# Optimization experiments

Hardware: AMD Instinct MI355X
Metric: run time of the kernel (lower is better)

## Reference

```python
import jax, jax.numpy as jnp
import numpy as np

H = W = 32
C = 384
NH = 12
HEAD = C // NH
SCALE = HEAD ** -0.5
WS = 8            # window size
SS = 4            # shift size
N = WS * WS       # tokens per window (64)
NW = (H // WS) * (W // WS)  # windows per image (16)
HIDDEN = 4 * C
EPS = 1e-5
SQRT_2_OVER_PI = float(np.sqrt(2.0 / np.pi))


def _relative_position_index():
    ch = np.arange(WS)
    coords = np.stack(np.meshgrid(ch, ch, indexing='ij')).reshape(2, -1)  # [2, N]
    rel = (coords[:, :, None] - coords[:, None, :]).transpose(1, 2, 0)    # [N, N, 2]
    rel[:, :, 0] += WS - 1
    rel[:, :, 1] += WS - 1
    rel[:, :, 0] *= 2 * WS - 1
    return rel.sum(-1)  # [N, N] int


def _attn_mask():
    img = np.zeros((H, W), np.float32)
    sl = (slice(0, -WS), slice(-WS, -SS), slice(-SS, None))
    cnt = 0
    for hs in sl:
        for ws_ in sl:
            img[hs, ws_] = cnt
            cnt += 1
    m = img.reshape(H // WS, WS, W // WS, WS).transpose(0, 2, 1, 3).reshape(-1, N)  # [nW, N]
    am = m[:, None, :] - m[:, :, None]
    return np.where(am != 0, -100.0, 0.0).astype(np.float32)  # [nW, N, N]


REL_IDX = jnp.asarray(_relative_position_index())
ATTN_MASK = jnp.asarray(_attn_mask())


def _gelu(x):
    return x * 0.5 * (1.0 + jnp.tanh(SQRT_2_OVER_PI * (x + 0.044715 * x ** 3)))


def _layernorm(x, g, b):
    mu = jnp.mean(x, axis=-1, keepdims=True)
    var = jnp.mean(jnp.square(x - mu), axis=-1, keepdims=True)
    return (x - mu) * jax.lax.rsqrt(var + EPS) * g + b


def _window_partition(x):  # [B,H,W,C] -> [B*nW, N, C]
    B = x.shape[0]
    x = x.reshape(B, H // WS, WS, W // WS, WS, C).transpose(0, 1, 3, 2, 4, 5)
    return x.reshape(-1, N, C)


def _window_reverse(w, B):  # [B*nW, N, C] -> [B,H,W,C]
    x = w.reshape(B, H // WS, W // WS, WS, WS, C).transpose(0, 1, 3, 2, 4, 5)
    return x.reshape(B, H, W, C)


def setup_inputs() -> dict:
    key = jax.random.key(0)
    ks = jax.random.split(key, 16)
    s = 0.02
    return {
        'x': jax.random.normal(ks[0], (32, H * W, C), jnp.float32),
        'norm1_g': jnp.ones((C,), jnp.float32),
        'norm1_b': jnp.zeros((C,), jnp.float32),
        'qkv_w': jax.random.normal(ks[1], (C, 3 * C), jnp.float32) * s,
        'qkv_b': jnp.zeros((3 * C,), jnp.float32),
        'rel_bias_table': jax.random.normal(ks[2], ((2 * WS - 1) ** 2, NH), jnp.float32) * s,
        'proj_w': jax.random.normal(ks[3], (C, C), jnp.float32) * s,
        'proj_b': jnp.zeros((C,), jnp.float32),
        'norm2_g': jnp.ones((C,), jnp.float32),
        'norm2_b': jnp.zeros((C,), jnp.float32),
        'fc1_w': jax.random.normal(ks[4], (C, HIDDEN), jnp.float32) * s,
        'fc1_b': jnp.zeros((HIDDEN,), jnp.float32),
        'fc2_w': jax.random.normal(ks[5], (HIDDEN, C), jnp.float32) * s,
        'fc2_b': jnp.zeros((C,), jnp.float32),
    }


def reference(x, norm1_g, norm1_b, qkv_w, qkv_b, rel_bias_table, proj_w, proj_b,
              norm2_g, norm2_b, fc1_w, fc1_b, fc2_w, fc2_b):
    B = x.shape[0]
    shortcut = x
    y = _layernorm(x, norm1_g, norm1_b).reshape(B, H, W, C)
    y = jnp.roll(y, shift=(-SS, -SS), axis=(1, 2))          # cyclic shift
    win = _window_partition(y)                               # [B*nW, N, C]

    qkv = (win @ qkv_w + qkv_b).reshape(-1, N, 3, NH, HEAD).transpose(2, 0, 3, 1, 4)
    q, k, v = qkv[0], qkv[1], qkv[2]                         # [B*nW, NH, N, HEAD]
    attn = jnp.einsum('whnd,whmd->whnm', q * SCALE, k)       # [B*nW, NH, N, N]

    bias = rel_bias_table[REL_IDX.reshape(-1)].reshape(N, N, NH).transpose(2, 0, 1)
    attn = attn + bias[None]
    attn = attn.reshape(B, NW, NH, N, N) + ATTN_MASK[None, :, None]
    attn = jax.nn.softmax(attn.reshape(-1, NH, N, N), axis=-1)

    out = jnp.einsum('whnm,whmd->wnhd', attn, v).reshape(-1, N, C)
    out = out @ proj_w + proj_b                              # [B*nW, N, C]

    y = _window_reverse(out, B)
    y = jnp.roll(y, shift=(SS, SS), axis=(1, 2)).reshape(B, H * W, C)

    x = shortcut + y                                         # drop_path is identity (eval)
    h = _layernorm(x, norm2_g, norm2_b)
    h = _gelu(h @ fc1_w + fc1_b) @ fc2_w + fc2_b
    return x + h
```

## Files before the change

kernel.cpp:

```cpp
#include <hip/hip_runtime.h>
#include <hip/hip_bf16.h>
#include <math.h>

typedef __hip_bfloat16 bf16;
typedef __attribute__((ext_vector_type(8))) short short8;
typedef __attribute__((ext_vector_type(4))) float floatx4;

static constexpr int TOK = 32768;
static constexpr int CDIM = 384;
static constexpr int HID = 1536;

__device__ __forceinline__ bf16 f2bf(float v) { return __float2bfloat16(v); }

__device__ __forceinline__ void unpack8(uint4 u, float* f) {
  f[0] = __uint_as_float(u.x << 16); f[1] = __uint_as_float(u.x & 0xffff0000u);
  f[2] = __uint_as_float(u.y << 16); f[3] = __uint_as_float(u.y & 0xffff0000u);
  f[4] = __uint_as_float(u.z << 16); f[5] = __uint_as_float(u.z & 0xffff0000u);
  f[6] = __uint_as_float(u.w << 16); f[7] = __uint_as_float(u.w & 0xffff0000u);
}

__device__ __forceinline__ unsigned short bf_bits(float a) {
  bf16 h = __float2bfloat16(a);
  unsigned short u;
  __builtin_memcpy(&u, &h, 2);
  return u;
}
__device__ __forceinline__ unsigned pack2(float a, float b) {
  return (unsigned)bf_bits(a) | ((unsigned)bf_bits(b) << 16);
}

typedef const __attribute__((address_space(1))) unsigned gas_t;
typedef __attribute__((address_space(3))) unsigned las_t;
__device__ __forceinline__ void gload16(const bf16* g, const bf16* l) {
  __builtin_amdgcn_global_load_lds((gas_t*)g, (las_t*)l, 16, 0, 0);
}

__global__ void k_convt(const float* __restrict__ src, bf16* __restrict__ dst,
                        int Kd, int Nd) {
  int tid = blockIdx.x * 256 + threadIdx.x;
  if (tid >= Kd * Nd) return;
  int k = tid / Nd, n = tid - k * Nd;
  dst[(size_t)n * Kd + k] = f2bf(src[tid]);
}

__global__ __launch_bounds__(256) void k_ln1(const float* __restrict__ x,
                                             const float* __restrict__ g,
                                             const float* __restrict__ b,
                                             bf16* __restrict__ out) {
  int wt = blockIdx.x * 4 + (threadIdx.x >> 6);
  int lane = threadIdx.x & 63;
  int win = wt >> 6, ntok = wt & 63;
  int bimg = win >> 4, wi = win & 15;
  int sh = (((wi >> 2) << 3) + (ntok >> 3) + 4) & 31;
  int sw = (((wi & 3) << 3) + (ntok & 7) + 4) & 31;
  const float* xr = x + ((size_t)bimg * 1024 + sh * 32 + sw) * CDIM;
  float v[6]; float s = 0.f, ss = 0.f;
#pragma unroll
  for (int j = 0; j < 6; ++j) {
    float t = xr[j * 64 + lane];
    v[j] = t; s += t; ss += t * t;
  }
#pragma unroll
  for (int off = 32; off > 0; off >>= 1) {
    s += __shfl_xor(s, off, 64);
    ss += __shfl_xor(ss, off, 64);
  }
  float mu = s * (1.f / 384.f);
  float var = ss * (1.f / 384.f) - mu * mu;
  float rs = rsqrtf(var + 1e-5f);
  bf16* orow = out + (size_t)wt * CDIM;
#pragma unroll
  for (int j = 0; j < 6; ++j) {
    int c = j * 64 + lane;
    orow[c] = f2bf((v[j] - mu) * rs * g[c] + b[c]);
  }
}

__global__ __launch_bounds__(256) void k_ln2(const float* __restrict__ x1,
                                             const float* __restrict__ g,
                                             const float* __restrict__ b,
                                             bf16* __restrict__ out) {
  int t = blockIdx.x * 4 + (threadIdx.x >> 6);
  int lane = threadIdx.x & 63;
  const float* xr = x1 + (size_t)t * CDIM;
  float v[6]; float s = 0.f, ss = 0.f;
#pragma unroll
  for (int j = 0; j < 6; ++j) {
    float q = xr[j * 64 + lane];
    v[j] = q; s += q; ss += q * q;
  }
#pragma unroll
  for (int off = 32; off > 0; off >>= 1) {
    s += __shfl_xor(s, off, 64);
    ss += __shfl_xor(ss, off, 64);
  }
  float mu = s * (1.f / 384.f);
  float var = ss * (1.f / 384.f) - mu * mu;
  float rs = rsqrtf(var + 1e-5f);
  bf16* orow = out + (size_t)t * CDIM;
#pragma unroll
  for (int j = 0; j < 6; ++j) {
    int c = j * 64 + lane;
    orow[c] = f2bf((v[j] - mu) * rs * g[c] + b[c]);
  }
}

template <int K, int EPI, int NT>
__global__ __launch_bounds__(256) void k_gemm(const bf16* __restrict__ A,
                                              const bf16* __restrict__ Bt,
                                              const float* __restrict__ bias,
                                              const float* __restrict__ extra,
                                              void* __restrict__ outp) {
  __shared__ __attribute__((aligned(16))) char pool[32768];
  bf16* As = (bf16*)pool;
  bf16* Bs = (bf16*)(pool + 16384);

  const int tid = threadIdx.x;
  const int wv = tid >> 6, lane = tid & 63;

  const int flat = blockIdx.x;
  const int xcd = flat & 7;
  const int idx = flat >> 3;
  const int rpx = (gridDim.x >> 3) / NT;
  const int cb = idx % NT;
  const int rb = idx / NT;
  const int mblk = (xcd * rpx + rb) * 128, nblk = cb * 128;

  const int srow = lane >> 3;
  const int scol8 = (lane & 7) ^ srow;
  const bf16* gaw = A + (size_t)(mblk + wv * 32 + srow) * K + scol8 * 8;
  const bf16* gbw = Bt + (size_t)(nblk + wv * 32 + srow) * K + scol8 * 8;
  const bf16* lAw = As + wv * 2048;
  const bf16* lBw = Bs + wv * 2048;

  const int wr = wv >> 1, wc = wv & 1;
  const int mr = lane & 15, q = lane >> 4;
  const bf16* faRow = As + (wr * 64 + mr) * 64;
  const bf16* fbRow = Bs + (wc * 64 + mr) * 64;
  const int sw0 = (q ^ (mr & 7)) * 8;
  const int sw4 = ((q + 4) ^ (mr & 7)) * 8;

  floatx4 acc[4][4];
#pragma unroll
  for (int i = 0; i < 4; ++i)
#pragma unroll
    for (int j = 0; j < 4; ++j) acc[i][j] = floatx4{0.f, 0.f, 0.f, 0.f};

  for (int k0 = 0; k0 < K; k0 += 64) {
    __syncthreads();
#pragma unroll
    for (int c = 0; c < 4; ++c) gload16(gaw + k0 + c * 8 * K, lAw + c * 512);
#pragma unroll
    for (int c = 0; c < 4; ++c) gload16(gbw + k0 + c * 8 * K, lBw + c * 512);
    __syncthreads();
    {
      short8 a[4], b[4];
#pragma unroll
      for (int mt = 0; mt < 4; ++mt) a[mt] = *(const short8*)(faRow + mt * 1024 + sw0);
#pragma unroll
      for (int nt = 0; nt < 4; ++nt) b[nt] = *(const short8*)(fbRow + nt * 1024 + sw0);
#pragma unroll
      for (int mt = 0; mt < 4; ++mt)
#pragma unroll
        for (int nt = 0; nt < 4; ++nt)
          acc[mt][nt] = __builtin_amdgcn_mfma_f32_16x16x32_bf16(a[mt], b[nt], acc[mt][nt], 0, 0, 0);
    }
    {
      short8 a[4], b[4];
#pragma unroll
      for (int mt = 0; mt < 4; ++mt) a[mt] = *(const short8*)(faRow + mt * 1024 + sw4);
#pragma unroll
      for (int nt = 0; nt < 4; ++nt) b[nt] = *(const short8*)(fbRow + nt * 1024 + sw4);
#pragma unroll
      for (int mt = 0; mt < 4; ++mt)
#pragma unroll
        for (int nt = 0; nt < 4; ++nt)
          acc[mt][nt] = __builtin_amdgcn_mfma_f32_16x16x32_bf16(a[mt], b[nt], acc[mt][nt], 0, 0, 0);
    }
  }

  __syncthreads();
  float* epsw = (float*)pool + wv * (16 * 68);
  const int rr = lane >> 2, c0 = (lane & 3) * 16;
#pragma unroll
  for (int mt = 0; mt < 4; ++mt) {
#pragma unroll
    for (int nt = 0; nt < 4; ++nt)
#pragma unroll
      for (int r = 0; r < 4; ++r)
        epsw[(q * 4 + r) * 68 + nt * 16 + mr] = acc[mt][nt][r];
    float v[16];
#pragma unroll
    for (int j = 0; j < 4; ++j) {
      float4 t = *(const float4*)&epsw[rr * 68 + c0 + j * 4];
      v[j * 4 + 0] = t.x; v[j * 4 + 1] = t.y; v[j * 4 + 2] = t.z; v[j * 4 + 3] = t.w;
    }
    const int grow = mblk + wr * 64 + mt * 16 + rr;
    const int gcol = nblk + wc * 64 + c0;

    if constexpr (EPI == 0) {
      int win = grow >> 6, ntok = grow & 63;
      int s = gcol / 384;
      int rem = gcol - s * 384;
      int h = rem >> 5, d0 = rem & 31;
      bf16* op = (bf16*)outp + (((size_t)s * 512 + win) * 12 + h) * 2048 + ntok * 32 + d0;
      uint4 pk;
      float bv[16];
#pragma unroll
      for (int j = 0; j < 16; ++j) bv[j] = v[j] + bias[gcol + j];
      pk.x = pack2(bv[0], bv[1]); pk.y = pack2(bv[2], bv[3]);
      pk.z = pack2(bv[4], bv[5]); pk.w = pack2(bv[6], bv[7]);
      *(uint4*)op = pk;
      pk.x = pack2(bv[8], bv[9]); pk.y = pack2(bv[10], bv[11]);
      pk.z = pack2(bv[12], bv[13]); pk.w = pack2(bv[14], bv[15]);
      *(uint4*)(op + 8) = pk;
    } else if constexpr (EPI == 1) {
      int win = grow >> 6, ntok = grow & 63;
      int bimg = win >> 4, wi = win & 15;
      int hh = (((wi >> 2) << 3) + (ntok >> 3) + 4) & 31;
      int ww = (((wi & 3) << 3) + (ntok & 7) + 4) & 31;
      size_t t = (size_t)bimg * 1024 + hh * 32 + ww;
      float* op = (float*)outp + t * CDIM + gcol;
      const float* xr = extra + t * CDIM + gcol;
#pragma unroll
      for (int j = 0; j < 4; ++j) {
        float4 xv = *(const float4*)(xr + j * 4);
        float4 ov;
        ov.x = xv.x + v[j * 4 + 0] + bias[gcol + j * 4 + 0];
        ov.y = xv.y + v[j * 4 + 1] + bias[gcol + j * 4 + 1];
        ov.z = xv.z + v[j * 4 + 2] + bias[gcol + j * 4 + 2];
        ov.w = xv.w + v[j * 4 + 3] + bias[gcol + j * 4 + 3];
        *(float4*)(op + j * 4) = ov;
      }
    } else if constexpr (EPI == 2) {
      float gv[16];
#pragma unroll
      for (int j = 0; j < 16; ++j) {
        float z = v[j] + bias[gcol + j];
        float u = 0.7978845608028654f * (z + 0.044715f * z * z * z);
        gv[j] = z / (1.f + __expf(-2.f * u));
      }
      bf16* op = (bf16*)outp + (size_t)grow * HID + gcol;
      uint4 pk;
      pk.x = pack2(gv[0], gv[1]); pk.y = pack2(gv[2], gv[3]);
      pk.z = pack2(gv[4], gv[5]); pk.w = pack2(gv[6], gv[7]);
      *(uint4*)op = pk;
      pk.x = pack2(gv[8], gv[9]); pk.y = pack2(gv[10], gv[11]);
      pk.z = pack2(gv[12], gv[13]); pk.w = pack2(gv[14], gv[15]);
      *(uint4*)(op + 8) = pk;
    } else {
      float* op = (float*)outp + (size_t)grow * CDIM + gcol;
      const float* xr = extra + (size_t)grow * CDIM + gcol;
#pragma unroll
      for (int j = 0; j < 4; ++j) {
        float4 xv = *(const float4*)(xr + j * 4);
        float4 ov;
        ov.x = xv.x + v[j * 4 + 0] + bias[gcol + j * 4 + 0];
        ov.y = xv.y + v[j * 4 + 1] + bias[gcol + j * 4 + 1];
        ov.z = xv.z + v[j * 4 + 2] + bias[gcol + j * 4 + 2];
        ov.w = xv.w + v[j * 4 + 3] + bias[gcol + j * 4 + 3];
        *(float4*)(op + j * 4) = ov;
      }
    }
  }
}

__global__ __launch_bounds__(64) void k_attn(const bf16* __restrict__ qkv,
                                             const float* __restrict__ tblg,
                                             bf16* __restrict__ out) {
  __shared__ __attribute__((aligned(16))) float ks[64][36];
  __shared__ __attribute__((aligned(16))) float vs[64][36];
  __shared__ float tbl[228];
  int bid = blockIdx.x;
  int win = bid / 12, head = bid - win * 12;
  int lane = threadIdx.x;

  for (int i = lane; i < 225; i += 64) tbl[i] = tblg[i * 12 + head];

  size_t base = ((size_t)win * 12 + head) * 2048 + lane * 32;
  const uint4* qp = (const uint4*)(qkv + base);
  const uint4* kp = (const uint4*)(qkv + (size_t)12582912 + base);
  const uint4* vp = (const uint4*)(qkv + (size_t)25165824 + base);

  float qreg[32];
#pragma unroll
  for (int i = 0; i < 4; ++i) { uint4 u = qp[i]; unpack8(u, qreg + i * 8); }
#pragma unroll
  for (int i = 0; i < 4; ++i) {
    uint4 u = kp[i]; float f[8]; unpack8(u, f);
    *(float4*)&ks[lane][i * 8] = make_float4(f[0], f[1], f[2], f[3]);
    *(float4*)&ks[lane][i * 8 + 4] = make_float4(f[4], f[5], f[6], f[7]);
  }
#pragma unroll
  for (int i = 0; i < 4; ++i) {
    uint4 u = vp[i]; float f[8]; unpack8(u, f);
    *(float4*)&vs[lane][i * 8] = make_float4(f[0], f[1], f[2], f[3]);
    *(float4*)&vs[lane][i * 8 + 4] = make_float4(f[4], f[5], f[6], f[7]);
  }

  int wi = win & 15;
  int r_i = lane >> 3, c_i = lane & 7;
  int rh = ((wi >> 2) << 3) + r_i, rw = ((wi & 3) << 3) + c_i;
  int rid = (rh < 24 ? 0 : (rh < 28 ? 1 : 2)) * 3 + (rw < 24 ? 0 : (rw < 28 ? 1 : 2));
  unsigned long long mask = 0;
#pragma unroll
  for (int v = 0; v < 9; ++v) {
    unsigned long long bb = __ballot(rid == v);
    if (rid == v) mask = bb;
  }
  const int base_i = r_i * 15 + c_i;
  __syncthreads();

  float o[32];
#pragma unroll
  for (int d = 0; d < 32; ++d) o[d] = 0.f;
  float l = 0.f;
#pragma unroll 2
  for (int j = 0; j < 64; ++j) {
    const float4* kr = (const float4*)ks[j];
    float dot = 0.f;
#pragma unroll
    for (int d4 = 0; d4 < 8; ++d4) {
      float4 kk = kr[d4];
      dot += qreg[d4 * 4 + 0] * kk.x;
      dot += qreg[d4 * 4 + 1] * kk.y;
      dot += qreg[d4 * 4 + 2] * kk.z;
      dot += qreg[d4 * 4 + 3] * kk.w;
    }
    int off_j = 112 - (j >> 3) * 15 - (j & 7);
    float bias = tbl[base_i + off_j];
    float madd = ((mask >> j) & 1ull) ? 0.f : -100.f;
    float p = __expf(dot * 0.17677669529663687f + bias + madd);
    l += p;
    const float4* vr = (const float4*)vs[j];
#pragma unroll
    for (int d4 = 0; d4 < 8; ++d4) {
      float4 vv = vr[d4];
      o[d4 * 4 + 0] += p * vv.x;
      o[d4 * 4 + 1] += p * vv.y;
      o[d4 * 4 + 2] += p * vv.z;
      o[d4 * 4 + 3] += p * vv.w;
    }
  }
  float inv = 1.f / l;
  uint4* o4 = (uint4*)(out + ((size_t)win * 64 + lane) * CDIM + head * 32);
#pragma unroll
  for (int i = 0; i < 4; ++i) {
    uint4 pk;
    pk.x = pack2(o[i * 8 + 0] * inv, o[i * 8 + 1] * inv);
    pk.y = pack2(o[i * 8 + 2] * inv, o[i * 8 + 3] * inv);
    pk.z = pack2(o[i * 8 + 4] * inv, o[i * 8 + 5] * inv);
    pk.w = pack2(o[i * 8 + 6] * inv, o[i * 8 + 7] * inv);
    o4[i] = pk;
  }
}

extern "C" void kernel_launch(void* const* d_in, const int* in_sizes, int n_in,
                              void* d_out, int out_size, void* d_ws, size_t ws_size,
                              hipStream_t stream) {
  const float* x = (const float*)d_in[0];
  const float* n1g = (const float*)d_in[1];
  const float* n1b = (const float*)d_in[2];
  const float* qkv_w = (const float*)d_in[3];
  const float* qkv_b = (const float*)d_in[4];
  const float* reltbl = (const float*)d_in[5];
  const float* proj_w = (const float*)d_in[6];
  const float* proj_b = (const float*)d_in[7];
  const float* n2g = (const float*)d_in[8];
  const float* n2b = (const float*)d_in[9];
  const float* fc1_w = (const float*)d_in[10];
  const float* fc1_b = (const float*)d_in[11];
  const float* fc2_w = (const float*)d_in[12];
  const float* fc2_b = (const float*)d_in[13];
  float* out = (float*)d_out;

  char* p = (char*)d_ws;
  bf16* w_qkv_t = (bf16*)p;  p += (size_t)442368 * 2;
  bf16* w_proj_t = (bf16*)p; p += (size_t)147456 * 2;
  bf16* w_fc1_t = (bf16*)p;  p += (size_t)589824 * 2;
  bf16* w_fc2_t = (bf16*)p;  p += (size_t)589824 * 2;
  bf16* bufA = (bf16*)p;     p += (size_t)12582912 * 2;
  bf16* qkvb = (bf16*)p;     p += (size_t)37748736 * 2;
  bf16* attno = (bf16*)p;    p += (size_t)12582912 * 2;
  float* x1 = (float*)p;     p += (size_t)12582912 * 4;
  bf16* hidden = qkvb;

  k_convt<<<dim3((442368 + 255) / 256), dim3(256), 0, stream>>>(qkv_w, w_qkv_t, 384, 1152);
  k_convt<<<dim3((147456 + 255) / 256), dim3(256), 0, stream>>>(proj_w, w_proj_t, 384, 384);
  k_convt<<<dim3((589824 + 255) / 256), dim3(256), 0, stream>>>(fc1_w, w_fc1_t, 384, 1536);
  k_convt<<<dim3((589824 + 255) / 256), dim3(256), 0, stream>>>(fc2_w, w_fc2_t, 1536, 384);

  k_ln1<<<dim3(8192), dim3(256), 0, stream>>>(x, n1g, n1b, bufA);
  k_gemm<384, 0, 9><<<dim3(9 * 256), dim3(256), 0, stream>>>(bufA, w_qkv_t, qkv_b, nullptr, qkvb);
  k_attn<<<dim3(6144), dim3(64), 0, stream>>>(qkvb, reltbl, attno);
  k_gemm<384, 1, 3><<<dim3(3 * 256), dim3(256), 0, stream>>>(attno, w_proj_t, proj_b, x, x1);
  k_ln2<<<dim3(8192), dim3(256), 0, stream>>>(x1, n2g, n2b, bufA);
  k_gemm<384, 2, 12><<<dim3(12 * 256), dim3(256), 0, stream>>>(bufA, w_fc1_t, fc1_b, nullptr, hidden);
  k_gemm<1536, 3, 3><<<dim3(3 * 256), dim3(256), 0, stream>>>(hidden, w_fc2_t, fc2_b, x1, out);
}
```

Measured before the change: 448.9 us.

## Rewrite window attention kernel with bf16 MFMA for QK^T and PV

The per-window attention kernel moves from per-lane scalar fp32 dot products over LDS-held K/V to bf16 MFMA 16x16x32 instructions for both the score and the output matmuls. Q, K and a transposed V are staged in LDS as bf16. Probabilities are written back to LDS as bf16, and row sums are reduced with shuffles. The aim is to cut the ALU-bound FMA work in attention, at the cost of bf16 rounding of the probabilities. Masked entries are zeroed directly instead of adding a -100 bias, and the code relies on single-wave ordering instead of barriers.

```diff
diff --git a/kernel.cpp b/kernel.cpp
--- a/kernel.cpp
+++ b/kernel.cpp
@@ -11,13 +11,6 @@
 static constexpr int HID = 1536;
 
 __device__ __forceinline__ bf16 f2bf(float v) { return __float2bfloat16(v); }
-
-__device__ __forceinline__ void unpack8(uint4 u, float* f) {
-  f[0] = __uint_as_float(u.x << 16); f[1] = __uint_as_float(u.x & 0xffff0000u);
-  f[2] = __uint_as_float(u.y << 16); f[3] = __uint_as_float(u.y & 0xffff0000u);
-  f[4] = __uint_as_float(u.z << 16); f[5] = __uint_as_float(u.z & 0xffff0000u);
-  f[6] = __uint_as_float(u.w << 16); f[7] = __uint_as_float(u.w & 0xffff0000u);
-}
 
 __device__ __forceinline__ unsigned short bf_bits(float a) {
   bf16 h = __float2bfloat16(a);
@@ -268,12 +261,19 @@
 __global__ __launch_bounds__(64) void k_attn(const bf16* __restrict__ qkv,
                                              const float* __restrict__ tblg,
                                              bf16* __restrict__ out) {
-  __shared__ __attribute__((aligned(16))) float ks[64][36];
-  __shared__ __attribute__((aligned(16))) float vs[64][36];
-  __shared__ float tbl[228];
-  int bid = blockIdx.x;
-  int win = bid / 12, head = bid - win * 12;
-  int lane = threadIdx.x;
+  __shared__ __attribute__((aligned(16))) char pool[16384];
+  bf16* Qs = (bf16*)pool;
+  bf16* Ks = (bf16*)(pool + 5120);
+  bf16* Ps = (bf16*)pool;
+  float* Os = (float*)pool;
+  bf16* Vt = (bf16*)(pool + 10240);
+  unsigned long long* msk = (unsigned long long*)(pool + 14848);
+  float* tbl = (float*)(pool + 15360);
+
+  const int bid = blockIdx.x;
+  const int win = bid / 12, head = bid - win * 12;
+  const int lane = threadIdx.x;
+  const int q = lane >> 4, mr = lane & 15;
 
   for (int i = lane; i < 225; i += 64) tbl[i] = tblg[i * 12 + head];
 
@@ -281,76 +281,131 @@
   const uint4* qp = (const uint4*)(qkv + base);
   const uint4* kp = (const uint4*)(qkv + (size_t)12582912 + base);
   const uint4* vp = (const uint4*)(qkv + (size_t)25165824 + base);
-
-  float qreg[32];
-#pragma unroll
-  for (int i = 0; i < 4; ++i) { uint4 u = qp[i]; unpack8(u, qreg + i * 8); }
-#pragma unroll
-  for (int i = 0; i < 4; ++i) {
-    uint4 u = kp[i]; float f[8]; unpack8(u, f);
-    *(float4*)&ks[lane][i * 8] = make_float4(f[0], f[1], f[2], f[3]);
-    *(float4*)&ks[lane][i * 8 + 4] = make_float4(f[4], f[5], f[6], f[7]);
-  }
-#pragma unroll
-  for (int i = 0; i < 4; ++i) {
-    uint4 u = vp[i]; float f[8]; unpack8(u, f);
-    *(float4*)&vs[lane][i * 8] = make_float4(f[0], f[1], f[2], f[3]);
-    *(float4*)&vs[lane][i * 8 + 4] = make_float4(f[4], f[5], f[6], f[7]);
-  }
-
-  int wi = win & 15;
-  int r_i = lane >> 3, c_i = lane & 7;
-  int rh = ((wi >> 2) << 3) + r_i, rw = ((wi & 3) << 3) + c_i;
-  int rid = (rh < 24 ? 0 : (rh < 28 ? 1 : 2)) * 3 + (rw < 24 ? 0 : (rw < 28 ? 1 : 2));
-  unsigned long long mask = 0;
-#pragma unroll
-  for (int v = 0; v < 9; ++v) {
-    unsigned long long bb = __ballot(rid == v);
-    if (rid == v) mask = bb;
-  }
-  const int base_i = r_i * 15 + c_i;
-  __syncthreads();
-
-  float o[32];
-#pragma unroll
-  for (int d = 0; d < 32; ++d) o[d] = 0.f;
-  float l = 0.f;
-#pragma unroll 2
-  for (int j = 0; j < 64; ++j) {
-    const float4* kr = (const float4*)ks[j];
-    float dot = 0.f;
-#pragma unroll
-    for (int d4 = 0; d4 < 8; ++d4) {
-      float4 kk = kr[d4];
-      dot += qreg[d4 * 4 + 0] * kk.x;
-      dot += qreg[d4 * 4 + 1] * kk.y;
-      dot += qreg[d4 * 4 + 2] * kk.z;
-      dot += qreg[d4 * 4 + 3] * kk.w;
-    }
-    int off_j = 112 - (j >> 3) * 15 - (j & 7);
-    float bias = tbl[base_i + off_j];
-    float madd = ((mask >> j) & 1ull) ? 0.f : -100.f;
-    float p = __expf(dot * 0.17677669529663687f + bias + madd);
-    l += p;
-    const float4* vr = (const float4*)vs[j];
-#pragma unroll
-    for (int d4 = 0; d4 < 8; ++d4) {
-      float4 vv = vr[d4];
-      o[d4 * 4 + 0] += p * vv.x;
-      o[d4 * 4 + 1] += p * vv.y;
-      o[d4 * 4 + 2] += p * vv.z;
-      o[d4 * 4 + 3] += p * vv.w;
-    }
-  }
-  float inv = 1.f / l;
+#pragma unroll
+  for (int i = 0; i < 4; ++i) *(uint4*)(Qs + lane * 40 + i * 8) = qp[i];
+#pragma unroll
+  for (int i = 0; i < 4; ++i) *(uint4*)(Ks + lane * 40 + i * 8) = kp[i];
+  {
+    union { uint4 u[4]; unsigned short h[32]; } vv;
+#pragma unroll
+    for (int i = 0; i < 4; ++i) vv.u[i] = vp[i];
+    unsigned short* VtU = (unsigned short*)Vt;
+#pragma unroll
+    for (int d = 0; d < 32; ++d) VtU[d * 72 + lane] = vv.h[d];
+  }
+  {
+    int wi = win & 15;
+    int ri = lane >> 3, ci = lane & 7;
+    int rh = ((wi >> 2) << 3) + ri, rw = ((wi & 3) << 3) + ci;
+    int rid = (rh < 24 ? 0 : (rh < 28 ? 1 : 2)) * 3 + (rw < 24 ? 0 : (rw < 28 ? 1 : 2));
+    unsigned long long m = 0;
+#pragma unroll
+    for (int v = 0; v < 9; ++v) {
+      unsigned long long bb = __ballot(rid == v);
+      if (rid == v) m = bb;
+    }
+    msk[lane] = m;
+  }
+
+  floatx4 sac[4][4];
+#pragma unroll
+  for (int i = 0; i < 4; ++i)
+#pragma unroll
+    for (int j = 0; j < 4; ++j) sac[i][j] = floatx4{0.f, 0.f, 0.f, 0.f};
+  {
+    short8 af[4], bf[4];
+#pragma unroll
+    for (int t = 0; t < 4; ++t) af[t] = *(const short8*)(Qs + (t * 16 + mr) * 40 + q * 8);
+#pragma unroll
+    for (int t = 0; t < 4; ++t) bf[t] = *(const short8*)(Ks + (t * 16 + mr) * 40 + q * 8);
+#pragma unroll
+    for (int mt = 0; mt < 4; ++mt)
+#pragma unroll
+      for (int nt = 0; nt < 4; ++nt)
+        sac[mt][nt] = __builtin_amdgcn_mfma_f32_16x16x32_bf16(af[mt], bf[nt], sac[mt][nt], 0, 0, 0);
+  }
+
+  float psum[4][4];
+#pragma unroll
+  for (int mt = 0; mt < 4; ++mt)
+#pragma unroll
+    for (int r = 0; r < 4; ++r) psum[mt][r] = 0.f;
+#pragma unroll
+  for (int mt = 0; mt < 4; ++mt) {
+#pragma unroll
+    for (int r = 0; r < 4; ++r) {
+      const int i = mt * 16 + q * 4 + r;
+      const unsigned long long mrow = msk[i];
+      const int bi = (i >> 3) * 15 + (i & 7);
+#pragma unroll
+      for (int nt = 0; nt < 4; ++nt) {
+        const int j = nt * 16 + mr;
+        const int idx = bi + 112 - (j >> 3) * 15 - (j & 7);
+        float val = sac[mt][nt][r] * 0.17677669529663687f + tbl[idx];
+        float p = __expf(val);
+        p = ((mrow >> j) & 1ull) ? p : 0.f;
+        psum[mt][r] += p;
+        Ps[i * 72 + j] = f2bf(p);
+      }
+    }
+  }
+  float inv[4][4];
+#pragma unroll
+  for (int mt = 0; mt < 4; ++mt)
+#pragma unroll
+    for (int r = 0; r < 4; ++r) {
+      float s = psum[mt][r];
+      s += __shfl_xor(s, 1, 64);
+      s += __shfl_xor(s, 2, 64);
+      s += __shfl_xor(s, 4, 64);
+      s += __shfl_xor(s, 8, 64);
+      inv[mt][r] = 1.f / s;
+    }
+
+  floatx4 oac[4][2];
+#pragma unroll
+  for (int i = 0; i < 4; ++i)
+#pragma unroll
+    for (int j = 0; j < 2; ++j) oac[i][j] = floatx4{0.f, 0.f, 0.f, 0.f};
+#pragma unroll
+  for (int kk = 0; kk < 2; ++kk) {
+    short8 ap[4], bv[2];
+#pragma unroll
+    for (int mt = 0; mt < 4; ++mt)
+      ap[mt] = *(const short8*)(Ps + (mt * 16 + mr) * 72 + kk * 32 + q * 8);
+#pragma unroll
+    for (int nt = 0; nt < 2; ++nt)
+      bv[nt] = *(const short8*)(Vt + (nt * 16 + mr) * 72 + kk * 32 + q * 8);
+#pragma unroll
+    for (int mt = 0; mt < 4; ++mt)
+#pragma unroll
+      for (int nt = 0; nt < 2; ++nt)
+        oac[mt][nt] = __builtin_amdgcn_mfma_f32_16x16x32_bf16(ap[mt], bv[nt], oac[mt][nt], 0, 0, 0);
+  }
+
+#pragma unroll
+  for (int mt = 0; mt < 4; ++mt)
+#pragma unroll
+    for (int nt = 0; nt < 2; ++nt)
+#pragma unroll
+      for (int r = 0; r < 4; ++r)
+        Os[(mt * 16 + q * 4 + r) * 40 + nt * 16 + mr] = oac[mt][nt][r] * inv[mt][r];
+  float ov[32];
+#pragma unroll
+  for (int c = 0; c < 8; ++c) {
+    const int cc = c ^ (lane & 7);
+    float4 t = *(const float4*)(Os + lane * 40 + cc * 4);
+    ov[cc * 4 + 0] = t.x; ov[cc * 4 + 1] = t.y;
+    ov[cc * 4 + 2] = t.z; ov[cc * 4 + 3] = t.w;
+  }
   uint4* o4 = (uint4*)(out + ((size_t)win * 64 + lane) * CDIM + head * 32);
 #pragma unroll
   for (int i = 0; i < 4; ++i) {
     uint4 pk;
-    pk.x = pack2(o[i * 8 + 0] * inv, o[i * 8 + 1] * inv);
-    pk.y = pack2(o[i * 8 + 2] * inv, o[i * 8 + 3] * inv);
-    pk.z = pack2(o[i * 8 + 4] * inv, o[i * 8 + 5] * inv);
-    pk.w = pack2(o[i * 8 + 6] * inv, o[i * 8 + 7] * inv);
+    pk.x = pack2(ov[i * 8 + 0], ov[i * 8 + 1]);
+    pk.y = pack2(ov[i * 8 + 2], ov[i * 8 + 3]);
+    pk.z = pack2(ov[i * 8 + 4], ov[i * 8 + 5]);
+    pk.w = pack2(ov[i * 8 + 6], ov[i * 8 + 7]);
     o4[i] = pk;
   }
 }
```

Result: faster. 435.8 us (-2.9%).
